# Kernel optimization log

Hardware: AMD Instinct MI355X
Metric: run time of the kernel (lower is better)

## Reference

```python
import jax, jax.numpy as jnp
import numpy as np

NUM_CLASSES = 21
EPS = 1e-6


def setup_inputs() -> dict:
    key = jax.random.key(0)
    k1, k2, k3 = jax.random.split(key, 3)
    feats = jax.random.normal(k1, (8, 256, 64, 64), dtype=jnp.float32)
    preds = jax.random.normal(k2, (8, NUM_CLASSES, 256, 256), dtype=jnp.float32)
    # labels in [0, 22): includes nclass=21 which acts as an ignore label
    masks = jax.random.randint(k3, (8, 256, 256), 0, 22, dtype=jnp.int64)
    return {"feats": feats, "preds": preds, "masks": masks}


def reference(feats, preds, masks):
    B, C = feats.shape[0], feats.shape[1]
    H, W = masks.shape[-2:]
    K = NUM_CLASSES

    # argmax over class logits -> predicted label map [B, H, W]
    pred_lbl = jnp.argmax(preds, axis=1)

    # bilinear upsample (align_corners=False, matches half-pixel resize)
    feats_up = jax.image.resize(feats, (B, C, H, W), method="bilinear")

    cls = jnp.arange(K)
    # one-hot of gt mask and of predictions; labels >= K (incl. 255) fall in
    # the dropped last channel of one_hot_2d, i.e. match no class here.
    gt_oh = (masks[:, None, :, :] == cls[None, :, None, None])      # [B,K,H,W]
    pr_oh = (pred_lbl[:, None, :, :] == cls[None, :, None, None])   # [B,K,H,W]
    joint = (gt_oh & pr_oh).astype(feats_up.dtype)                  # [B,K,H,W]

    counts = joint.sum(axis=(2, 3))                                  # [B,K]
    sums = jnp.einsum("bchw,bkhw->bkc", feats_up, joint)            # [B,K,C]

    # per-image class means (absent classes -> 0/eps = 0), then batch mean
    proto = (sums / (counts[..., None] + EPS)).mean(axis=0)          # [K,C]
    return proto
```

## Files before the change

kernel.cpp:

```cpp
#include <hip/hip_runtime.h>

#define KC   21
#define BB   8
#define CC   256
#define HWP  65536
#define SRC  4096
#define NS   64
#define PC   64

#define WSF_PARTW 131072
#define WSF_PART  (WSF_PARTW + BB*NS*KC)

__global__ __launch_bounds__(256, 2)
void k1_classify(const float* __restrict__ preds,
                 const int*   __restrict__ masks,
                 unsigned char* __restrict__ L,
                 float* __restrict__ out)
{
    int tid = threadIdx.x;
    if (blockIdx.x == 0) {
        float4* o4 = reinterpret_cast<float4*>(out);
#pragma unroll
        for (int i = 0; i < (KC * CC / 4 + 255) / 256; ++i) {
            int j = tid + i * 256;
            if (j < KC * CC / 4) o4[j] = make_float4(0.f, 0.f, 0.f, 0.f);
        }
    }

    int idx = blockIdx.x * 256 + tid;
    int b   = idx >> 14;
    int hw4 = (idx & 16383) << 2;

    const float* pb = preds + (size_t)b * KC * HWP + hw4;
    float va[4][KC];
#pragma unroll
    for (int k = 0; k < KC; ++k) {
        float4 t = *reinterpret_cast<const float4*>(pb + (size_t)k * HWP);
        va[0][k] = t.x; va[1][k] = t.y; va[2][k] = t.z; va[3][k] = t.w;
    }

    int4 mm = *reinterpret_cast<const int4*>(masks + b * HWP + hw4);
    int mk[4] = { mm.x, mm.y, mm.z, mm.w };

    uchar4 r;
    unsigned char* rp = reinterpret_cast<unsigned char*>(&r);
#pragma unroll
    for (int j = 0; j < 4; ++j) {
        float best = va[j][0];
        int   bi   = 0;
#pragma unroll
        for (int k = 1; k < KC; ++k) {
            if (va[j][k] > best) { best = va[j][k]; bi = k; }
        }
        rp[j] = (mk[j] == bi) ? (unsigned char)bi : (unsigned char)255;
    }
    *reinterpret_cast<uchar4*>(L + (size_t)b * HWP + hw4) = r;
}

__global__ __launch_bounds__(512, 4)
void k2_contract(const float* __restrict__ feats,
                 const unsigned char* __restrict__ L,
                 float* __restrict__ partial,
                 float* __restrict__ partialw)
{
    __shared__ float ws[KC * PC];
    __shared__ float scr[KC * CC];
    int s = blockIdx.x, b = blockIdx.y;
    int tid = threadIdx.x;
    int p0 = s * PC;

    int cp   = tid & 255;
    int psub = tid >> 8;
    int pw   = psub * 32;

    if (tid < KC * PC / 4)
        *reinterpret_cast<float4*>(ws + tid * 4) = make_float4(0.f, 0.f, 0.f, 0.f);

    float f[32];
    {
        const float* frow = feats + (size_t)(b * CC + cp) * SRC + p0 + pw;
#pragma unroll
        for (int q = 0; q < 8; ++q) {
            float4 t = *reinterpret_cast<const float4*>(frow + q * 4);
            f[q * 4 + 0] = t.x; f[q * 4 + 1] = t.y;
            f[q * 4 + 2] = t.z; f[q * 4 + 3] = t.w;
        }
    }
    __syncthreads();

    {
        int r = tid >> 6, cb = tid & 63;
        int h = 4 * s - 2 + r;
        if ((unsigned)h < 256u) {
            float sy = h * 0.25f - 0.375f;
            int   yt = (int)floorf(sy);
            float wy = sy - (float)yt;
            int ya = yt < 0 ? 0 : yt;
            int yb = yt + 1 > 63 ? 63 : yt + 1;
            float wyy = ((ya == s) ? (1.f - wy) : 0.f) + ((yb == s) ? wy : 0.f);
            if (wyy != 0.f) {
                const unsigned char* Lrow = L + ((size_t)b << 16) + ((size_t)h << 8);
#pragma unroll
                for (int j = 0; j < 4; ++j) {
                    int w = cb + j * 64;
                    int k = Lrow[w];
                    if (k < KC) {
                        float sx = w * 0.25f - 0.375f;
                        int   xt = (int)floorf(sx);
                        float wx = sx - (float)xt;
                        int xa = xt < 0 ? 0 : xt;
                        int xb = xt + 1 > 63 ? 63 : xt + 1;
                        atomicAdd(&ws[k * PC + xa], wyy * (1.f - wx));
                        atomicAdd(&ws[k * PC + xb], wyy * wx);
                    }
                }
            }
        }
    }
    __syncthreads();

    float swcnt = 0.f;
    if (tid < KC) {
#pragma unroll
        for (int p = 0; p < PC; ++p) swcnt += ws[tid * PC + ((p + tid * 3) & (PC - 1))];
    }

    float acc[KC];
#pragma unroll
    for (int k = 0; k < KC; ++k) {
        const float* wk = ws + k * PC + pw;
        float a0 = 0.f, a1 = 0.f, a2 = 0.f, a3 = 0.f;
#pragma unroll
        for (int q = 0; q < 8; ++q) {
            float4 w4 = *reinterpret_cast<const float4*>(wk + q * 4);
            a0 += w4.x * f[q * 4 + 0];
            a1 += w4.y * f[q * 4 + 1];
            a2 += w4.z * f[q * 4 + 2];
            a3 += w4.w * f[q * 4 + 3];
        }
        acc[k] = (a0 + a1) + (a2 + a3);
    }

    if (psub == 1) {
#pragma unroll
        for (int k = 0; k < KC; ++k) scr[k * CC + cp] = acc[k];
    }
    __syncthreads();
    if (psub == 0) {
        float* op = partial + ((size_t)(b * NS + s)) * KC * CC + cp;
#pragma unroll
        for (int k = 0; k < KC; ++k)
            op[(size_t)k * CC] = acc[k] + scr[k * CC + cp];
    }

    if (tid < KC)
        partialw[(size_t)(b * NS + s) * KC + tid] = swcnt;
}

__global__ __launch_bounds__(256)
void k3_finalize(const float* __restrict__ partial,
                 const float* __restrict__ partialw,
                 float* __restrict__ out)
{
    int k = blockIdx.x, b = blockIdx.y;
    int tid = threadIdx.x;

    const float* base = partial + ((size_t)(b * NS) * KC + k) * CC + tid;
    float acc = 0.f;
#pragma unroll 8
    for (int s = 0; s < NS; ++s) acc += base[(size_t)s * KC * CC];

    __shared__ float red;
    if (tid < 64) {
        float v = partialw[(size_t)(b * NS + tid) * KC + k];
#pragma unroll
        for (int off = 32; off; off >>= 1) v += __shfl_down(v, off);
        if (tid == 0) red = v;
    }
    __syncthreads();
    float cnt = red;

    atomicAdd(&out[k * CC + tid], acc / (8.f * (cnt + 1e-6f)));
}

extern "C" void kernel_launch(void* const* d_in, const int* in_sizes, int n_in,
                              void* d_out, int out_size, void* d_ws, size_t ws_size,
                              hipStream_t stream) {
    const float* feats = (const float*)d_in[0];
    const float* preds = (const float*)d_in[1];
    const int*   masks = (const int*)  d_in[2];
    float* out = (float*)d_out;

    float* wsf = (float*)d_ws;
    unsigned char* L = (unsigned char*)d_ws;
    float* partialw = wsf + WSF_PARTW;
    float* partial  = wsf + WSF_PART;

    k1_classify<<<(BB * HWP / 4) / 256, 256, 0, stream>>>(preds, masks, L, out);
    k2_contract<<<dim3(NS, BB), 512, 0, stream>>>(feats, L, partial, partialw);
    k3_finalize<<<dim3(KC, BB), 256, 0, stream>>>(partial, partialw, out);
}
```

Baseline: 33.35 us.

## Process two source rows per block in contraction kernel with 1024 threads

Each contraction block now covers two low-res feature rows (128 source pixels) using 1024 threads. This halves the number of blocks and the partial results that the finalize kernel must reduce. Bilinear weights for both rows are built from a shared 12-row window of label rows, reducing redundant label reads. The cost is a larger shared-memory scratch for the four-way reduction and fewer blocks, which may leave the GPU underfilled.

```diff
diff --git a/kernel.cpp b/kernel.cpp
--- a/kernel.cpp
+++ b/kernel.cpp
@@ -5,11 +5,11 @@
 #define CC   256
 #define HWP  65536
 #define SRC  4096
-#define NS   64
-#define PC   64
+#define NS   32
+#define PC   128
 
 #define WSF_PARTW 131072
-#define WSF_PART  (WSF_PARTW + BB*NS*KC)
+#define WSF_PART  139264
 
 __global__ __launch_bounds__(256, 2)
 void k1_classify(const float* __restrict__ preds,
@@ -57,24 +57,25 @@
     *reinterpret_cast<uchar4*>(L + (size_t)b * HWP + hw4) = r;
 }
 
-__global__ __launch_bounds__(512, 4)
+__global__ __launch_bounds__(1024, 4)
 void k2_contract(const float* __restrict__ feats,
                  const unsigned char* __restrict__ L,
                  float* __restrict__ partial,
                  float* __restrict__ partialw)
 {
     __shared__ float ws[KC * PC];
-    __shared__ float scr[KC * CC];
+    __shared__ float scr[3 * KC * CC];
     int s = blockIdx.x, b = blockIdx.y;
     int tid = threadIdx.x;
     int p0 = s * PC;
+    int ybase = 2 * s;
 
     int cp   = tid & 255;
     int psub = tid >> 8;
     int pw   = psub * 32;
 
-    if (tid < KC * PC / 4)
-        *reinterpret_cast<float4*>(ws + tid * 4) = make_float4(0.f, 0.f, 0.f, 0.f);
+    for (int t = tid; t < KC * PC / 4; t += 1024)
+        *reinterpret_cast<float4*>(ws + t * 4) = make_float4(0.f, 0.f, 0.f, 0.f);
 
     float f[32];
     {
@@ -90,15 +91,16 @@
 
     {
         int r = tid >> 6, cb = tid & 63;
-        int h = 4 * s - 2 + r;
-        if ((unsigned)h < 256u) {
+        int h = 8 * s - 2 + r;
+        if (r < 12 && (unsigned)h < 256u) {
             float sy = h * 0.25f - 0.375f;
             int   yt = (int)floorf(sy);
             float wy = sy - (float)yt;
             int ya = yt < 0 ? 0 : yt;
             int yb = yt + 1 > 63 ? 63 : yt + 1;
-            float wyy = ((ya == s) ? (1.f - wy) : 0.f) + ((yb == s) ? wy : 0.f);
-            if (wyy != 0.f) {
+            float wyy0 = ((ya == ybase)     ? (1.f - wy) : 0.f) + ((yb == ybase)     ? wy : 0.f);
+            float wyy1 = ((ya == ybase + 1) ? (1.f - wy) : 0.f) + ((yb == ybase + 1) ? wy : 0.f);
+            if (wyy0 != 0.f || wyy1 != 0.f) {
                 const unsigned char* Lrow = L + ((size_t)b << 16) + ((size_t)h << 8);
 #pragma unroll
                 for (int j = 0; j < 4; ++j) {
@@ -110,8 +112,15 @@
                         float wx = sx - (float)xt;
                         int xa = xt < 0 ? 0 : xt;
                         int xb = xt + 1 > 63 ? 63 : xt + 1;
-                        atomicAdd(&ws[k * PC + xa], wyy * (1.f - wx));
-                        atomicAdd(&ws[k * PC + xb], wyy * wx);
+                        float* wk = ws + k * PC;
+                        if (wyy0 != 0.f) {
+                            atomicAdd(wk + xa, wyy0 * (1.f - wx));
+                            atomicAdd(wk + xb, wyy0 * wx);
+                        }
+                        if (wyy1 != 0.f) {
+                            atomicAdd(wk + 64 + xa, wyy1 * (1.f - wx));
+                            atomicAdd(wk + 64 + xb, wyy1 * wx);
+                        }
                     }
                 }
             }
@@ -122,7 +131,8 @@
     float swcnt = 0.f;
     if (tid < KC) {
 #pragma unroll
-        for (int p = 0; p < PC; ++p) swcnt += ws[tid * PC + ((p + tid * 3) & (PC - 1))];
+        for (int i = 0; i < PC; ++i)
+            swcnt += ws[tid * PC + ((i + tid * 8) & (PC - 1))];
     }
 
     float acc[KC];
@@ -141,16 +151,21 @@
         acc[k] = (a0 + a1) + (a2 + a3);
     }
 
-    if (psub == 1) {
-#pragma unroll
-        for (int k = 0; k < KC; ++k) scr[k * CC + cp] = acc[k];
+    if (psub >= 1) {
+        float* sp = scr + (psub - 1) * (KC * CC);
+#pragma unroll
+        for (int k = 0; k < KC; ++k) sp[k * CC + cp] = acc[k];
     }
     __syncthreads();
     if (psub == 0) {
         float* op = partial + ((size_t)(b * NS + s)) * KC * CC + cp;
 #pragma unroll
-        for (int k = 0; k < KC; ++k)
-            op[(size_t)k * CC] = acc[k] + scr[k * CC + cp];
+        for (int k = 0; k < KC; ++k) {
+            float v = acc[k] + scr[k * CC + cp]
+                             + scr[KC * CC + k * CC + cp]
+                             + scr[2 * KC * CC + k * CC + cp];
+            op[(size_t)k * CC] = v;
+        }
     }
 
     if (tid < KC)
@@ -172,7 +187,7 @@
 
     __shared__ float red;
     if (tid < 64) {
-        float v = partialw[(size_t)(b * NS + tid) * KC + k];
+        float v = (tid < NS) ? partialw[(size_t)(b * NS + tid) * KC + k] : 0.f;
 #pragma unroll
         for (int off = 32; off; off >>= 1) v += __shfl_down(v, off);
         if (tid == 0) red = v;
@@ -197,6 +212,6 @@
     float* partial  = wsf + WSF_PART;
 
     k1_classify<<<(BB * HWP / 4) / 256, 256, 0, stream>>>(preds, masks, L, out);
-    k2_contract<<<dim3(NS, BB), 512, 0, stream>>>(feats, L, partial, partialw);
+    k2_contract<<<dim3(NS, BB), 1024, 0, stream>>>(feats, L, partial, partialw);
     k3_finalize<<<dim3(KC, BB), 256, 0, stream>>>(partial, partialw, out);
 }
```

New measurement: 32.10 us (median of 2 runs). -3.7%, faster.
